# Kernel optimization log

Hardware: AMD Instinct MI355X
Metric: run time of the kernel (lower is better)

Reference implementation:

```python
import jax, jax.numpy as jnp
import numpy as np

N = 50000      # nodes
E = 800000     # edges (before self-loops)
D_IN = 256     # input feature dim
H = 4          # attention heads
C = 32         # per-head channels
HID = H * C    # 128, concat output dim
BN_EPS = 1e-5


def setup_inputs() -> dict:
    key = jax.random.key(0)
    ks = jax.random.split(key, 24)
    inp = {}
    inp["x"] = jax.random.normal(ks[0], (N, D_IN), jnp.float32)
    inp["edge_index"] = jax.random.randint(ks[1], (2, E), 0, N, jnp.int32)
    # layer 1 GATConv params
    inp["W1"] = jax.random.normal(ks[2], (D_IN, HID), jnp.float32) * (2.0 / (D_IN + HID)) ** 0.5
    inp["att_src1"] = jax.random.normal(ks[3], (H, C), jnp.float32) * 0.1
    inp["att_dst1"] = jax.random.normal(ks[4], (H, C), jnp.float32) * 0.1
    inp["bias1"] = jnp.zeros((HID,), jnp.float32)
    # layer 1 BatchNorm (eval mode)
    inp["gamma1"] = 1.0 + 0.1 * jax.random.normal(ks[5], (HID,), jnp.float32)
    inp["beta1"] = 0.1 * jax.random.normal(ks[6], (HID,), jnp.float32)
    inp["mean1"] = 0.1 * jax.random.normal(ks[7], (HID,), jnp.float32)
    inp["var1"] = 0.5 + jax.random.uniform(ks[8], (HID,), jnp.float32)
    # layer 2 GATConv params
    inp["W2"] = jax.random.normal(ks[9], (HID, HID), jnp.float32) * (2.0 / (HID + HID)) ** 0.5
    inp["att_src2"] = jax.random.normal(ks[10], (H, C), jnp.float32) * 0.1
    inp["att_dst2"] = jax.random.normal(ks[11], (H, C), jnp.float32) * 0.1
    inp["bias2"] = jnp.zeros((HID,), jnp.float32)
    # layer 2 BatchNorm (eval mode)
    inp["gamma2"] = 1.0 + 0.1 * jax.random.normal(ks[12], (HID,), jnp.float32)
    inp["beta2"] = 0.1 * jax.random.normal(ks[13], (HID,), jnp.float32)
    inp["mean2"] = 0.1 * jax.random.normal(ks[14], (HID,), jnp.float32)
    inp["var2"] = 0.5 + jax.random.uniform(ks[15], (HID,), jnp.float32)
    return inp


def _gat_layer(x, src, dst, W, att_src, att_dst, bias):
    # x: [N, D]; src/dst: [Etot] with self-loops already appended
    h = (x @ W).reshape(N, H, C)                       # [N, H, C]
    a_s = jnp.einsum("nhc,hc->nh", h, att_src)         # [N, H]
    a_d = jnp.einsum("nhc,hc->nh", h, att_dst)         # [N, H]
    e = jax.nn.leaky_relu(a_s[src] + a_d[dst], 0.2)    # [Etot, H]
    # edge softmax over incoming edges of each destination node
    m = jax.ops.segment_max(e, dst, num_segments=N)    # [N, H]
    ex = jnp.exp(e - m[dst])                           # [Etot, H]
    den = jax.ops.segment_sum(ex, dst, num_segments=N) # [N, H]
    alpha = ex / (den[dst] + 1e-16)                    # [Etot, H]
    out = jax.ops.segment_sum(h[src] * alpha[:, :, None], dst, num_segments=N)
    return out.reshape(N, HID) + bias                  # concat heads + bias


def _bn_eval(x, gamma, beta, mean, var):
    return (x - mean) * (gamma * jax.lax.rsqrt(var + BN_EPS)) + beta


def reference(x, edge_index, W1, att_src1, att_dst1, bias1, gamma1, beta1, mean1, var1,
              W2, att_src2, att_dst2, bias2, gamma2, beta2, mean2, var2):
    loop = jnp.arange(N, dtype=edge_index.dtype)
    src = jnp.concatenate([edge_index[0], loop])  # PyG GATConv adds self-loops
    dst = jnp.concatenate([edge_index[1], loop])
    h = _gat_layer(x, src, dst, W1, att_src1, att_dst1, bias1)
    h = jax.nn.relu(_bn_eval(h, gamma1, beta1, mean1, var1))  # dropout = identity (eval)
    h = _gat_layer(h, src, dst, W2, att_src2, att_dst2, bias2)
    h = jax.nn.relu(_bn_eval(h, gamma2, beta2, mean2, var2))
    return h
```

## Files before the change

### kernel.cpp

```cpp
#include <hip/hip_runtime.h>
#include <math.h>

#define N_NODES 50000
#define EDGES   800000
#define ETOT    (EDGES + N_NODES)
#define HID     128
#define NH      4

typedef __attribute__((ext_vector_type(8))) short short8;
typedef __attribute__((ext_vector_type(4))) float floatx4;

__device__ inline unsigned short f2bf(float f) {
    unsigned int u = __float_as_uint(f);
    u = u + 0x7FFFu + ((u >> 16) & 1u);
    return (unsigned short)(u >> 16);
}

__device__ inline float sel4(float4 v, int h) {
    return h == 0 ? v.x : (h == 1 ? v.y : (h == 2 ? v.z : v.w));
}

#define NB 391
#define CHUNK 4096
#define BIN_BLOCKS ((ETOT + CHUNK - 1) / CHUNK)

__global__ __launch_bounds__(256) void bin_count_kernel(const int* __restrict__ ei,
                                                        int* __restrict__ histG) {
    __shared__ int histL[NB];
    int t = threadIdx.x;
    for (int b = t; b < NB; b += 256) histL[b] = 0;
    __syncthreads();
    int base = blockIdx.x * CHUNK;
#pragma unroll
    for (int j = 0; j < 16; j++) {
        int e = base + j * 256 + t;
        if (e < ETOT) {
            int d = (e < EDGES) ? ei[EDGES + e] : (e - EDGES);
            atomicAdd(&histL[d >> 7], 1);
        }
    }
    __syncthreads();
    for (int b = t; b < NB; b += 256) {
        int c = histL[b];
        if (c) atomicAdd(&histG[b], c);
    }
}

__global__ __launch_bounds__(512) void bucket_scan_kernel(const int* __restrict__ histG,
                                                          int* __restrict__ bucket_base,
                                                          int* __restrict__ bucket_cursor) {
    __shared__ int sh[512];
    int t = threadIdx.x;
    int v = (t < NB) ? histG[t] : 0;
    sh[t] = v;
    __syncthreads();
    for (int off = 1; off < 512; off <<= 1) {
        int x = sh[t];
        int add = (t >= off) ? sh[t - off] : 0;
        __syncthreads();
        sh[t] = x + add;
        __syncthreads();
    }
    if (t < NB) { int ex = sh[t] - v; bucket_base[t] = ex; bucket_cursor[t] = ex; }
    if (t == 511) bucket_base[NB] = sh[511];
}

__global__ __launch_bounds__(256) void bin_scatter_kernel(const int* __restrict__ ei,
                                                          int* __restrict__ bucket_cursor,
                                                          int2* __restrict__ binned) {
    __shared__ int histL[NB];
    int t = threadIdx.x;
    for (int b = t; b < NB; b += 256) histL[b] = 0;
    __syncthreads();
    int base = blockIdx.x * CHUNK;
#pragma unroll
    for (int j = 0; j < 16; j++) {
        int e = base + j * 256 + t;
        if (e < ETOT) {
            int d = (e < EDGES) ? ei[EDGES + e] : (e - EDGES);
            atomicAdd(&histL[d >> 7], 1);
        }
    }
    __syncthreads();
    for (int b = t; b < NB; b += 256) {
        int c = histL[b];
        histL[b] = c ? atomicAdd(&bucket_cursor[b], c) : 0;
    }
    __syncthreads();
#pragma unroll
    for (int j = 0; j < 16; j++) {
        int e = base + j * 256 + t;
        if (e < ETOT) {
            int s, d;
            if (e < EDGES) { s = ei[e]; d = ei[EDGES + e]; }
            else           { s = d = e - EDGES; }
            int pos = atomicAdd(&histL[d >> 7], 1);
            binned[pos] = make_int2(s, d);
        }
    }
}

__global__ __launch_bounds__(256) void bin_finalize_kernel(const int2* __restrict__ binned,
                                                           const int* __restrict__ bucket_base,
                                                           int* __restrict__ offsets,
                                                           int* __restrict__ csr) {
    __shared__ int histN[128];
    __shared__ int excl[128];
    int b = blockIdx.x, t = threadIdx.x;
    int n0 = b << 7;
    int ebase = bucket_base[b];
    int ecnt  = bucket_base[b + 1] - ebase;
    if (t < 128) histN[t] = 0;
    __syncthreads();
    for (int j = t; j < ecnt; j += 256)
        atomicAdd(&histN[binned[ebase + j].y - n0], 1);
    __syncthreads();
    int v = (t < 128) ? histN[t] : 0;
    if (t < 128) excl[t] = v;
    __syncthreads();
    for (int off = 1; off < 128; off <<= 1) {
        int x = 0, add = 0;
        if (t < 128) { x = excl[t]; if (t >= off) add = excl[t - off]; }
        __syncthreads();
        if (t < 128) excl[t] = x + add;
        __syncthreads();
    }
    if (t < 128) {
        int ex = excl[t] - v;
        int n = n0 + t;
        if (n < N_NODES) offsets[n] = ebase + ex;
        histN[t] = ex;
    }
    if (b == NB - 1 && t == 0) offsets[N_NODES] = ETOT;
    __syncthreads();
    for (int j = t; j < ecnt; j += 256) {
        int2 e = binned[ebase + j];
        int pos = atomicAdd(&histN[e.y - n0], 1);
        csr[ebase + pos] = e.x;
    }
}

__global__ void coef_kernel(const float* __restrict__ b1, const float* __restrict__ g1,
                            const float* __restrict__ be1, const float* __restrict__ mn1,
                            const float* __restrict__ vr1,
                            const float* __restrict__ b2, const float* __restrict__ g2,
                            const float* __restrict__ be2, const float* __restrict__ mn2,
                            const float* __restrict__ vr2, float* __restrict__ coef) {
    int t = threadIdx.x;
    if (t < 128) {
        float sc = g1[t] * rsqrtf(vr1[t] + 1e-5f);
        coef[t]       = sc;
        coef[128 + t] = be1[t] + (b1[t] - mn1[t]) * sc;
    } else {
        int c = t - 128;
        float sc = g2[c] * rsqrtf(vr2[c] + 1e-5f);
        coef[256 + c] = sc;
        coef[384 + c] = be2[c] + (b2[c] - mn2[c]) * sc;
    }
}

__global__ void wtrans_kernel(const float* __restrict__ W1, const float* __restrict__ W2,
                              unsigned short* __restrict__ Wt1, unsigned short* __restrict__ Wt2) {
    int i = blockIdx.x * 256 + threadIdx.x;
    if (i < 256 * 128) { int k = i >> 7, n = i & 127; Wt1[n * 256 + k] = f2bf(W1[i]); }
    if (i < 128 * 128) { int k = i >> 7, n = i & 127; Wt2[n * 128 + k] = f2bf(W2[i]); }
}

#define GR   128
#define KC   64
#define PADK 88
#define PADH 136

union Smem {
    struct { unsigned short Xs[GR][PADK]; unsigned short Ws[HID][PADK]; } s;
    unsigned short Hs[GR][PADH];
};

template<bool XBF16>
__global__ __launch_bounds__(256) void gemm_att_kernel(const void* __restrict__ Xv,
                                                       const unsigned short* __restrict__ Wt,
                                                       const float* __restrict__ att_src,
                                                       const float* __restrict__ att_dst,
                                                       unsigned short* __restrict__ Hout,
                                                       float* __restrict__ aS,
                                                       float* __restrict__ aD, int K) {
    __shared__ Smem sm;
    int t = threadIdx.x, lane = t & 63, w = t >> 6;
    int quad = lane >> 4, nl = lane & 15;
    int rowBase = blockIdx.x * GR;

    floatx4 acc[2][8];
    floatx4 zero = {0.f, 0.f, 0.f, 0.f};
#pragma unroll
    for (int a = 0; a < 2; a++)
#pragma unroll
        for (int b = 0; b < 8; b++) acc[a][b] = zero;

    const float*          Xf = (const float*)Xv;
    const unsigned short* Xb = (const unsigned short*)Xv;

    for (int k0 = 0; k0 < K; k0 += KC) {
#pragma unroll
        for (int it = 0; it < 4; it++) {
            int s5 = t + it * 256;
            int row = s5 >> 3, kg = s5 & 7;
            int gr = rowBase + row;
            unsigned short tmp[8];
            if (XBF16) {
                uint4 v = make_uint4(0, 0, 0, 0);
                if (gr < N_NODES) v = *(const uint4*)&Xb[(unsigned)(gr * K + k0 + kg * 8)];
                *(uint4*)tmp = v;
            } else {
                float4 v0 = make_float4(0, 0, 0, 0), v1 = v0;
                if (gr < N_NODES) {
                    const float* p = &Xf[(unsigned)(gr * K + k0 + kg * 8)];
                    v0 = *(const float4*)p;
                    v1 = *(const float4*)(p + 4);
                }
                tmp[0] = f2bf(v0.x); tmp[1] = f2bf(v0.y); tmp[2] = f2bf(v0.z); tmp[3] = f2bf(v0.w);
                tmp[4] = f2bf(v1.x); tmp[5] = f2bf(v1.y); tmp[6] = f2bf(v1.z); tmp[7] = f2bf(v1.w);
            }
            *(uint4*)&sm.s.Xs[row][kg * 8] = *(uint4*)tmp;
        }
#pragma unroll
        for (int it = 0; it < 4; it++) {
            int s5 = t + it * 256;
            int n = s5 >> 3, kg = s5 & 7;
            *(uint4*)&sm.s.Ws[n][kg * 8] = *(const uint4*)&Wt[(unsigned)(n * K + k0 + kg * 8)];
        }
        __syncthreads();
#pragma unroll
        for (int ks = 0; ks < 2; ks++) {
            int kb = ks * 32 + quad * 8;
            short8 a0 = *(const short8*)&sm.s.Xs[w * 32 + nl][kb];
            short8 a1 = *(const short8*)&sm.s.Xs[w * 32 + 16 + nl][kb];
#pragma unroll
            for (int ct = 0; ct < 8; ct++) {
                short8 b = *(const short8*)&sm.s.Ws[ct * 16 + nl][kb];
                acc[0][ct] = __builtin_amdgcn_mfma_f32_16x16x32_bf16(a0, b, acc[0][ct], 0, 0, 0);
                acc[1][ct] = __builtin_amdgcn_mfma_f32_16x16x32_bf16(a1, b, acc[1][ct], 0, 0, 0);
            }
        }
        __syncthreads();
    }

#pragma unroll
    for (int rt = 0; rt < 2; rt++)
#pragma unroll
        for (int ct = 0; ct < 8; ct++)
#pragma unroll
            for (int r = 0; r < 4; r++)
                sm.Hs[w * 32 + rt * 16 + quad * 4 + r][ct * 16 + nl] = f2bf(acc[rt][ct][r]);

    float asv[8], adv[8];
    {
        const float* ap = &att_src[nl * 8];
        const float* dp = &att_dst[nl * 8];
        *(float4*)&asv[0] = *(const float4*)ap;  *(float4*)&asv[4] = *(const float4*)(ap + 4);
        *(float4*)&adv[0] = *(const float4*)dp;  *(float4*)&adv[4] = *(const float4*)(dp + 4);
    }
    int hd = nl >> 2;
#pragma unroll
    for (int it = 0; it < 8; it++) {
        int rl = w * 32 + it * 4 + quad;
        int grow = rowBase + rl;
        uint4 v = *(const uint4*)&sm.Hs[rl][nl * 8];
        float f[8];
        f[0] = __uint_as_float(v.x << 16); f[1] = __uint_as_float(v.x & 0xffff0000u);
        f[2] = __uint_as_float(v.y << 16); f[3] = __uint_as_float(v.y & 0xffff0000u);
        f[4] = __uint_as_float(v.z << 16); f[5] = __uint_as_float(v.z & 0xffff0000u);
        f[6] = __uint_as_float(v.w << 16); f[7] = __uint_as_float(v.w & 0xffff0000u);
        float ds = 0.f, dd = 0.f;
#pragma unroll
        for (int j = 0; j < 8; j++) {
            ds = fmaf(f[j], asv[j], ds);
            dd = fmaf(f[j], adv[j], dd);
        }
        ds += __shfl_xor(ds, 1); ds += __shfl_xor(ds, 2);
        dd += __shfl_xor(dd, 1); dd += __shfl_xor(dd, 2);
        if (grow < N_NODES) {
            *(uint4*)&Hout[(unsigned)(grow * HID + nl * 8)] = v;
            if ((nl & 3) == 0) { aS[grow * 4 + hd] = ds; aD[grow * 4 + hd] = dd; }
        }
    }
}

#define ASTRIDE 132

template<bool OUTBF16>
__global__ __launch_bounds__(256) void gather_kernel(const unsigned short* __restrict__ hfeat,
                                                     const float* __restrict__ a_s,
                                                     const float* __restrict__ a_d,
                                                     const int* __restrict__ offsets,
                                                     const int* __restrict__ csr,
                                                     const float* __restrict__ coefA,
                                                     const float* __restrict__ coefB,
                                                     void* __restrict__ outv) {
    __shared__ float alphaT[4][4][ASTRIDE];
    __shared__ int   offS[4][128];
    int t = threadIdx.x, lane = t & 63, ws = t >> 6;
    int n = blockIdx.x * 4 + ws;
    int start = offsets[n], end = offsets[n + 1];
    int deg = end - start;
    float4 ad4 = *(const float4*)&a_d[(unsigned)(n * 4)];

    int i0 = start + lane, i1 = i0 + 64;
    bool v0 = lane < deg, v1 = lane + 64 < deg;
    int s0 = 0, s1 = 0;
    float e00 = -1e30f, e01 = -1e30f, e02 = -1e30f, e03 = -1e30f;
    float e10 = -1e30f, e11 = -1e30f, e12 = -1e30f, e13 = -1e30f;
    if (v0) {
        s0 = csr[i0];
        float4 as4 = *(const float4*)&a_s[(unsigned)(s0 * 4)];
        e00 = as4.x + ad4.x; e00 = e00 > 0.f ? e00 : 0.2f * e00;
        e01 = as4.y + ad4.y; e01 = e01 > 0.f ? e01 : 0.2f * e01;
        e02 = as4.z + ad4.z; e02 = e02 > 0.f ? e02 : 0.2f * e02;
        e03 = as4.w + ad4.w; e03 = e03 > 0.f ? e03 : 0.2f * e03;
    }
    if (v1) {
        s1 = csr[i1];
        float4 as4 = *(const float4*)&a_s[(unsigned)(s1 * 4)];
        e10 = as4.x + ad4.x; e10 = e10 > 0.f ? e10 : 0.2f * e10;
        e11 = as4.y + ad4.y; e11 = e11 > 0.f ? e11 : 0.2f * e11;
        e12 = as4.z + ad4.z; e12 = e12 > 0.f ? e12 : 0.2f * e12;
        e13 = as4.w + ad4.w; e13 = e13 > 0.f ? e13 : 0.2f * e13;
    }
    float m0 = fmaxf(e00, e10), m1 = fmaxf(e01, e11);
    float m2 = fmaxf(e02, e12), m3 = fmaxf(e03, e13);
    for (int i = start + 128 + lane; i < end; i += 64) {
        float4 as4 = *(const float4*)&a_s[(unsigned)(csr[i] * 4)];
        float f0 = as4.x + ad4.x; f0 = f0 > 0.f ? f0 : 0.2f * f0;
        float f1 = as4.y + ad4.y; f1 = f1 > 0.f ? f1 : 0.2f * f1;
        float f2 = as4.z + ad4.z; f2 = f2 > 0.f ? f2 : 0.2f * f2;
        float f3 = as4.w + ad4.w; f3 = f3 > 0.f ? f3 : 0.2f * f3;
        m0 = fmaxf(m0, f0); m1 = fmaxf(m1, f1);
        m2 = fmaxf(m2, f2); m3 = fmaxf(m3, f3);
    }
#pragma unroll
    for (int off = 32; off > 0; off >>= 1) {
        m0 = fmaxf(m0, __shfl_xor(m0, off));
        m1 = fmaxf(m1, __shfl_xor(m1, off));
        m2 = fmaxf(m2, __shfl_xor(m2, off));
        m3 = fmaxf(m3, __shfl_xor(m3, off));
    }
    float x00 = __expf(e00 - m0), x01 = __expf(e01 - m1);
    float x02 = __expf(e02 - m2), x03 = __expf(e03 - m3);
    float x10 = __expf(e10 - m0), x11 = __expf(e11 - m1);
    float x12 = __expf(e12 - m2), x13 = __expf(e13 - m3);
    float d0 = x00 + x10, d1 = x01 + x11, d2 = x02 + x12, d3 = x03 + x13;
    for (int i = start + 128 + lane; i < end; i += 64) {
        float4 as4 = *(const float4*)&a_s[(unsigned)(csr[i] * 4)];
        float f0 = as4.x + ad4.x; f0 = f0 > 0.f ? f0 : 0.2f * f0;
        float f1 = as4.y + ad4.y; f1 = f1 > 0.f ? f1 : 0.2f * f1;
        float f2 = as4.z + ad4.z; f2 = f2 > 0.f ? f2 : 0.2f * f2;
        float f3 = as4.w + ad4.w; f3 = f3 > 0.f ? f3 : 0.2f * f3;
        d0 += __expf(f0 - m0); d1 += __expf(f1 - m1);
        d2 += __expf(f2 - m2); d3 += __expf(f3 - m3);
    }
#pragma unroll
    for (int off = 32; off > 0; off >>= 1) {
        d0 += __shfl_xor(d0, off);
        d1 += __shfl_xor(d1, off);
        d2 += __shfl_xor(d2, off);
        d3 += __shfl_xor(d3, off);
    }
    float rd0 = 1.0f / (d0 + 1e-16f);
    float rd1 = 1.0f / (d1 + 1e-16f);
    float rd2 = 1.0f / (d2 + 1e-16f);
    float rd3 = 1.0f / (d3 + 1e-16f);

    if (v0) {
        alphaT[ws][0][lane] = x00 * rd0;
        alphaT[ws][1][lane] = x01 * rd1;
        alphaT[ws][2][lane] = x02 * rd2;
        alphaT[ws][3][lane] = x03 * rd3;
        offS[ws][lane] = s0 << 8;
    }
    if (v1) {
        alphaT[ws][0][lane + 64] = x10 * rd0;
        alphaT[ws][1][lane + 64] = x11 * rd1;
        alphaT[ws][2][lane + 64] = x12 * rd2;
        alphaT[ws][3][lane + 64] = x13 * rd3;
        offS[ws][lane + 64] = s1 << 8;
    }
    __syncthreads();

    int c = lane * 2;
    int h0 = lane >> 4;
    int lane4 = lane * 4;
    const char* hbase = (const char*)hfeat;
    float mh  = sel4(make_float4(m0, m1, m2, m3), h0);
    float rdh = sel4(make_float4(rd0, rd1, rd2, rd3), h0);
    float adh = sel4(ad4, h0);

    float acc0 = 0.f, acc1 = 0.f;
    int cap = deg < 128 ? deg : 128;
    int j = 0;
    for (; j + 3 < cap; j += 4) {
        unsigned oA = (unsigned)(offS[ws][j]     + lane4);
        unsigned oB = (unsigned)(offS[ws][j + 1] + lane4);
        unsigned oC = (unsigned)(offS[ws][j + 2] + lane4);
        unsigned oD = (unsigned)(offS[ws][j + 3] + lane4);
        float aA = alphaT[ws][h0][j],     aB = alphaT[ws][h0][j + 1];
        float aC = alphaT[ws][h0][j + 2], aD2 = alphaT[ws][h0][j + 3];
        unsigned int vA = *(const unsigned int*)(hbase + oA);
        unsigned int vB = *(const unsigned int*)(hbase + oB);
        unsigned int vC = *(const unsigned int*)(hbase + oC);
        unsigned int vD = *(const unsigned int*)(hbase + oD);
        acc0 = fmaf(__uint_as_float(vA << 16),         aA,  acc0);
        acc1 = fmaf(__uint_as_float(vA & 0xffff0000u), aA,  acc1);
        acc0 = fmaf(__uint_as_float(vB << 16),         aB,  acc0);
        acc1 = fmaf(__uint_as_float(vB & 0xffff0000u), aB,  acc1);
        acc0 = fmaf(__uint_as_float(vC << 16),         aC,  acc0);
        acc1 = fmaf(__uint_as_float(vC & 0xffff0000u), aC,  acc1);
        acc0 = fmaf(__uint_as_float(vD << 16),         aD2, acc0);
        acc1 = fmaf(__uint_as_float(vD & 0xffff0000u), aD2, acc1);
    }
    for (; j < cap; j++) {
        unsigned o = (unsigned)(offS[ws][j] + lane4);
        float al = alphaT[ws][h0][j];
        unsigned int v = *(const unsigned int*)(hbase + o);
        acc0 = fmaf(__uint_as_float(v << 16),         al, acc0);
        acc1 = fmaf(__uint_as_float(v & 0xffff0000u), al, acc1);
    }
    for (; j < deg; j++) {
        int s = csr[start + j];
        float as = a_s[(unsigned)(s * 4 + h0)];
        float e = as + adh; e = e > 0.f ? e : 0.2f * e;
        float al = __expf(e - mh) * rdh;
        unsigned int v = *(const unsigned int*)(hbase + (unsigned)((s << 8) + lane4));
        acc0 = fmaf(__uint_as_float(v << 16),         al, acc0);
        acc1 = fmaf(__uint_as_float(v & 0xffff0000u), al, acc1);
    }
    float2 cA = *(const float2*)&coefA[c];
    float2 cB = *(const float2*)&coefB[c];
    float o0 = fmaxf(fmaf(acc0, cA.x, cB.x), 0.f);
    float o1 = fmaxf(fmaf(acc1, cA.y, cB.y), 0.f);
    if (OUTBF16) {
        unsigned int pk = (unsigned int)f2bf(o0) | ((unsigned int)f2bf(o1) << 16);
        ((unsigned int*)outv)[(unsigned)(n * 64 + lane)] = pk;
    } else {
        ((float2*)outv)[(unsigned)(n * 64 + lane)] = make_float2(o0, o1);
    }
}

extern "C" void kernel_launch(void* const* d_in, const int* in_sizes, int n_in,
                              void* d_out, int out_size, void* d_ws, size_t ws_size,
                              hipStream_t stream) {
    const float* x    = (const float*)d_in[0];
    const int*   ei   = (const int*)d_in[1];
    const float* W1   = (const float*)d_in[2];
    const float* as1  = (const float*)d_in[3];
    const float* ad1  = (const float*)d_in[4];
    const float* b1   = (const float*)d_in[5];
    const float* g1   = (const float*)d_in[6];
    const float* be1  = (const float*)d_in[7];
    const float* mn1  = (const float*)d_in[8];
    const float* vr1  = (const float*)d_in[9];
    const float* W2   = (const float*)d_in[10];
    const float* as2  = (const float*)d_in[11];
    const float* ad2  = (const float*)d_in[12];
    const float* b2   = (const float*)d_in[13];
    const float* g2   = (const float*)d_in[14];
    const float* be2  = (const float*)d_in[15];
    const float* mn2  = (const float*)d_in[16];
    const float* vr2  = (const float*)d_in[17];
    float* out = (float*)d_out;

    unsigned short* hb  = (unsigned short*)d_ws;
    unsigned short* x2b = hb + (size_t)N_NODES * HID;
    unsigned short* Wt1 = x2b + (size_t)N_NODES * HID;
    unsigned short* Wt2 = Wt1 + 128 * 256;
    float* aS    = (float*)(Wt2 + 128 * 128);
    float* aD    = aS + N_NODES * NH;
    float* coef  = aD + N_NODES * NH;
    int* histG         = (int*)(coef + 512);
    int* bucket_base   = histG + NB;
    int* bucket_cursor = bucket_base + NB + 1;
    int* offsets       = bucket_cursor + NB;
    int2* binned       = (int2*)(offsets + N_NODES + 1);
    int* csr           = (int*)(binned + ETOT);

    hipMemsetAsync(histG, 0, NB * sizeof(int), stream);
    bin_count_kernel<<<BIN_BLOCKS, 256, 0, stream>>>(ei, histG);
    bucket_scan_kernel<<<1, 512, 0, stream>>>(histG, bucket_base, bucket_cursor);
    bin_scatter_kernel<<<BIN_BLOCKS, 256, 0, stream>>>(ei, bucket_cursor, binned);
    bin_finalize_kernel<<<NB, 256, 0, stream>>>(binned, bucket_base, offsets, csr);
    coef_kernel<<<1, 256, 0, stream>>>(b1, g1, be1, mn1, vr1, b2, g2, be2, mn2, vr2, coef);
    wtrans_kernel<<<128, 256, 0, stream>>>(W1, W2, Wt1, Wt2);

    int gemmGrid = (N_NODES + GR - 1) / GR;
    int nodeGrid = N_NODES / 4;

    gemm_att_kernel<false><<<gemmGrid, 256, 0, stream>>>(x, Wt1, as1, ad1, hb, aS, aD, 256);
    gather_kernel<true><<<nodeGrid, 256, 0, stream>>>(hb, aS, aD, offsets, csr,
                                                      coef, coef + 128, (void*)x2b);
    gemm_att_kernel<true><<<gemmGrid, 256, 0, stream>>>(x2b, Wt2, as2, ad2, hb, aS, aD, 128);
    gather_kernel<false><<<nodeGrid, 256, 0, stream>>>(hb, aS, aD, offsets, csr,
                                                       coef + 256, coef + 384, (void*)out);
}
```

Measured before the change: 282.4 us.

## Split edge-softmax across heads per 16-lane group and unroll gather by eight

The softmax phase now assigns each 16-lane quarter of the wavefront to one head, so each lane handles single-head logits for up to 64 cached edges instead of all four heads for 128 edges. This cuts per-lane register use and shortens the shuffle reductions to 4 steps. The shared-memory cache shrinks to 64 edges, and the aggregation loop is unrolled by 8 so more independent feature loads are in flight. Nodes with degree above 64 now fall back more often to the slower recompute path, and a_s is read once per head per edge rather than once as a float4.

```diff
diff --git a/kernel.cpp b/kernel.cpp
--- a/kernel.cpp
+++ b/kernel.cpp
@@ -14,10 +14,6 @@
     unsigned int u = __float_as_uint(f);
     u = u + 0x7FFFu + ((u >> 16) & 1u);
     return (unsigned short)(u >> 16);
-}
-
-__device__ inline float sel4(float4 v, int h) {
-    return h == 0 ? v.x : (h == 1 ? v.y : (h == 2 ? v.z : v.w));
 }
 
 #define NB 391
@@ -285,7 +281,8 @@
     }
 }
 
-#define ASTRIDE 132
+#define ECAP 64
+#define ASTRIDE 68
 
 template<bool OUTBF16>
 __global__ __launch_bounds__(256) void gather_kernel(const unsigned short* __restrict__ hfeat,
@@ -297,137 +294,95 @@
                                                      const float* __restrict__ coefB,
                                                      void* __restrict__ outv) {
     __shared__ float alphaT[4][4][ASTRIDE];
-    __shared__ int   offS[4][128];
+    __shared__ int   offS[4][ECAP];
     int t = threadIdx.x, lane = t & 63, ws = t >> 6;
+    int h = lane >> 4, l16 = lane & 15;
     int n = blockIdx.x * 4 + ws;
     int start = offsets[n], end = offsets[n + 1];
     int deg = end - start;
-    float4 ad4 = *(const float4*)&a_d[(unsigned)(n * 4)];
-
-    int i0 = start + lane, i1 = i0 + 64;
-    bool v0 = lane < deg, v1 = lane + 64 < deg;
-    int s0 = 0, s1 = 0;
-    float e00 = -1e30f, e01 = -1e30f, e02 = -1e30f, e03 = -1e30f;
-    float e10 = -1e30f, e11 = -1e30f, e12 = -1e30f, e13 = -1e30f;
-    if (v0) {
-        s0 = csr[i0];
-        float4 as4 = *(const float4*)&a_s[(unsigned)(s0 * 4)];
-        e00 = as4.x + ad4.x; e00 = e00 > 0.f ? e00 : 0.2f * e00;
-        e01 = as4.y + ad4.y; e01 = e01 > 0.f ? e01 : 0.2f * e01;
-        e02 = as4.z + ad4.z; e02 = e02 > 0.f ? e02 : 0.2f * e02;
-        e03 = as4.w + ad4.w; e03 = e03 > 0.f ? e03 : 0.2f * e03;
-    }
-    if (v1) {
-        s1 = csr[i1];
-        float4 as4 = *(const float4*)&a_s[(unsigned)(s1 * 4)];
-        e10 = as4.x + ad4.x; e10 = e10 > 0.f ? e10 : 0.2f * e10;
-        e11 = as4.y + ad4.y; e11 = e11 > 0.f ? e11 : 0.2f * e11;
-        e12 = as4.z + ad4.z; e12 = e12 > 0.f ? e12 : 0.2f * e12;
-        e13 = as4.w + ad4.w; e13 = e13 > 0.f ? e13 : 0.2f * e13;
-    }
-    float m0 = fmaxf(e00, e10), m1 = fmaxf(e01, e11);
-    float m2 = fmaxf(e02, e12), m3 = fmaxf(e03, e13);
-    for (int i = start + 128 + lane; i < end; i += 64) {
-        float4 as4 = *(const float4*)&a_s[(unsigned)(csr[i] * 4)];
-        float f0 = as4.x + ad4.x; f0 = f0 > 0.f ? f0 : 0.2f * f0;
-        float f1 = as4.y + ad4.y; f1 = f1 > 0.f ? f1 : 0.2f * f1;
-        float f2 = as4.z + ad4.z; f2 = f2 > 0.f ? f2 : 0.2f * f2;
-        float f3 = as4.w + ad4.w; f3 = f3 > 0.f ? f3 : 0.2f * f3;
-        m0 = fmaxf(m0, f0); m1 = fmaxf(m1, f1);
-        m2 = fmaxf(m2, f2); m3 = fmaxf(m3, f3);
-    }
-#pragma unroll
-    for (int off = 32; off > 0; off >>= 1) {
-        m0 = fmaxf(m0, __shfl_xor(m0, off));
-        m1 = fmaxf(m1, __shfl_xor(m1, off));
-        m2 = fmaxf(m2, __shfl_xor(m2, off));
-        m3 = fmaxf(m3, __shfl_xor(m3, off));
-    }
-    float x00 = __expf(e00 - m0), x01 = __expf(e01 - m1);
-    float x02 = __expf(e02 - m2), x03 = __expf(e03 - m3);
-    float x10 = __expf(e10 - m0), x11 = __expf(e11 - m1);
-    float x12 = __expf(e12 - m2), x13 = __expf(e13 - m3);
-    float d0 = x00 + x10, d1 = x01 + x11, d2 = x02 + x12, d3 = x03 + x13;
-    for (int i = start + 128 + lane; i < end; i += 64) {
-        float4 as4 = *(const float4*)&a_s[(unsigned)(csr[i] * 4)];
-        float f0 = as4.x + ad4.x; f0 = f0 > 0.f ? f0 : 0.2f * f0;
-        float f1 = as4.y + ad4.y; f1 = f1 > 0.f ? f1 : 0.2f * f1;
-        float f2 = as4.z + ad4.z; f2 = f2 > 0.f ? f2 : 0.2f * f2;
-        float f3 = as4.w + ad4.w; f3 = f3 > 0.f ? f3 : 0.2f * f3;
-        d0 += __expf(f0 - m0); d1 += __expf(f1 - m1);
-        d2 += __expf(f2 - m2); d3 += __expf(f3 - m3);
-    }
-#pragma unroll
-    for (int off = 32; off > 0; off >>= 1) {
-        d0 += __shfl_xor(d0, off);
-        d1 += __shfl_xor(d1, off);
-        d2 += __shfl_xor(d2, off);
-        d3 += __shfl_xor(d3, off);
-    }
-    float rd0 = 1.0f / (d0 + 1e-16f);
-    float rd1 = 1.0f / (d1 + 1e-16f);
-    float rd2 = 1.0f / (d2 + 1e-16f);
-    float rd3 = 1.0f / (d3 + 1e-16f);
-
-    if (v0) {
-        alphaT[ws][0][lane] = x00 * rd0;
-        alphaT[ws][1][lane] = x01 * rd1;
-        alphaT[ws][2][lane] = x02 * rd2;
-        alphaT[ws][3][lane] = x03 * rd3;
-        offS[ws][lane] = s0 << 8;
-    }
-    if (v1) {
-        alphaT[ws][0][lane + 64] = x10 * rd0;
-        alphaT[ws][1][lane + 64] = x11 * rd1;
-        alphaT[ws][2][lane + 64] = x12 * rd2;
-        alphaT[ws][3][lane + 64] = x13 * rd3;
-        offS[ws][lane + 64] = s1 << 8;
+    float adh = a_d[(unsigned)(n * 4 + h)];
+
+    float e[4];
+    int   sreg[4];
+#pragma unroll
+    for (int it = 0; it < 4; it++) {
+        int j = l16 + it * 16;
+        e[it] = -1e30f;
+        if (j < deg) {
+            int s = csr[start + j];
+            sreg[it] = s;
+            float as = a_s[(unsigned)(s * 4 + h)];
+            float v = as + adh;
+            e[it] = v > 0.f ? v : 0.2f * v;
+        }
+    }
+    float m = fmaxf(fmaxf(e[0], e[1]), fmaxf(e[2], e[3]));
+    for (int j = ECAP + l16; j < deg; j += 16) {
+        int s = csr[start + j];
+        float as = a_s[(unsigned)(s * 4 + h)];
+        float v = as + adh; v = v > 0.f ? v : 0.2f * v;
+        m = fmaxf(m, v);
+    }
+#pragma unroll
+    for (int off = 1; off < 16; off <<= 1) m = fmaxf(m, __shfl_xor(m, off));
+
+    float x[4];
+    float d = 0.f;
+#pragma unroll
+    for (int it = 0; it < 4; it++) { x[it] = __expf(e[it] - m); d += x[it]; }
+    for (int j = ECAP + l16; j < deg; j += 16) {
+        int s = csr[start + j];
+        float as = a_s[(unsigned)(s * 4 + h)];
+        float v = as + adh; v = v > 0.f ? v : 0.2f * v;
+        d += __expf(v - m);
+    }
+#pragma unroll
+    for (int off = 1; off < 16; off <<= 1) d += __shfl_xor(d, off);
+    float rd = 1.0f / (d + 1e-16f);
+
+#pragma unroll
+    for (int it = 0; it < 4; it++) {
+        int j = l16 + it * 16;
+        if (j < deg) {
+            alphaT[ws][h][j] = x[it] * rd;
+            if (h == 0) offS[ws][j] = sreg[it] << 8;
+        }
     }
     __syncthreads();
 
     int c = lane * 2;
-    int h0 = lane >> 4;
     int lane4 = lane * 4;
     const char* hbase = (const char*)hfeat;
-    float mh  = sel4(make_float4(m0, m1, m2, m3), h0);
-    float rdh = sel4(make_float4(rd0, rd1, rd2, rd3), h0);
-    float adh = sel4(ad4, h0);
 
     float acc0 = 0.f, acc1 = 0.f;
-    int cap = deg < 128 ? deg : 128;
+    int cap = deg < ECAP ? deg : ECAP;
     int j = 0;
-    for (; j + 3 < cap; j += 4) {
-        unsigned oA = (unsigned)(offS[ws][j]     + lane4);
-        unsigned oB = (unsigned)(offS[ws][j + 1] + lane4);
-        unsigned oC = (unsigned)(offS[ws][j + 2] + lane4);
-        unsigned oD = (unsigned)(offS[ws][j + 3] + lane4);
-        float aA = alphaT[ws][h0][j],     aB = alphaT[ws][h0][j + 1];
-        float aC = alphaT[ws][h0][j + 2], aD2 = alphaT[ws][h0][j + 3];
-        unsigned int vA = *(const unsigned int*)(hbase + oA);
-        unsigned int vB = *(const unsigned int*)(hbase + oB);
-        unsigned int vC = *(const unsigned int*)(hbase + oC);
-        unsigned int vD = *(const unsigned int*)(hbase + oD);
-        acc0 = fmaf(__uint_as_float(vA << 16),         aA,  acc0);
-        acc1 = fmaf(__uint_as_float(vA & 0xffff0000u), aA,  acc1);
-        acc0 = fmaf(__uint_as_float(vB << 16),         aB,  acc0);
-        acc1 = fmaf(__uint_as_float(vB & 0xffff0000u), aB,  acc1);
-        acc0 = fmaf(__uint_as_float(vC << 16),         aC,  acc0);
-        acc1 = fmaf(__uint_as_float(vC & 0xffff0000u), aC,  acc1);
-        acc0 = fmaf(__uint_as_float(vD << 16),         aD2, acc0);
-        acc1 = fmaf(__uint_as_float(vD & 0xffff0000u), aD2, acc1);
+    for (; j + 7 < cap; j += 8) {
+        unsigned o[8]; float a[8]; unsigned v[8];
+#pragma unroll
+        for (int u = 0; u < 8; u++) o[u] = (unsigned)(offS[ws][j + u] + lane4);
+#pragma unroll
+        for (int u = 0; u < 8; u++) a[u] = alphaT[ws][h][j + u];
+#pragma unroll
+        for (int u = 0; u < 8; u++) v[u] = *(const unsigned int*)(hbase + o[u]);
+#pragma unroll
+        for (int u = 0; u < 8; u++) {
+            acc0 = fmaf(__uint_as_float(v[u] << 16),         a[u], acc0);
+            acc1 = fmaf(__uint_as_float(v[u] & 0xffff0000u), a[u], acc1);
+        }
     }
     for (; j < cap; j++) {
         unsigned o = (unsigned)(offS[ws][j] + lane4);
-        float al = alphaT[ws][h0][j];
+        float al = alphaT[ws][h][j];
         unsigned int v = *(const unsigned int*)(hbase + o);
         acc0 = fmaf(__uint_as_float(v << 16),         al, acc0);
         acc1 = fmaf(__uint_as_float(v & 0xffff0000u), al, acc1);
     }
     for (; j < deg; j++) {
         int s = csr[start + j];
-        float as = a_s[(unsigned)(s * 4 + h0)];
-        float e = as + adh; e = e > 0.f ? e : 0.2f * e;
-        float al = __expf(e - mh) * rdh;
+        float as = a_s[(unsigned)(s * 4 + h)];
+        float v2 = as + adh; v2 = v2 > 0.f ? v2 : 0.2f * v2;
+        float al = __expf(v2 - m) * rd;
         unsigned int v = *(const unsigned int*)(hbase + (unsigned)((s << 8) + lane4));
         acc0 = fmaf(__uint_as_float(v << 16),         al, acc0);
         acc1 = fmaf(__uint_as_float(v & 0xffff0000u), al, acc1);
```

Measured after the change: 282.9 us. No clear change (+0.2%).
